# Optimization experiments

Measured on AMD Instinct MI355X. Metric: run time of the kernel, lower is better.

## Reference

```python
import jax, jax.numpy as jnp
import numpy as np

B, D, T, K = 32, 64, 4096, 512
COMMITMENT_COST = 0.25


def setup_inputs() -> dict:
    key = jax.random.key(0)
    k1, k2 = jax.random.split(key)
    z = jax.random.normal(k1, (B, D, T), dtype=jnp.float32)
    # nn.Embedding init: uniform(-1/K, 1/K)
    codebook = jax.random.uniform(k2, (K, D), dtype=jnp.float32,
                                  minval=-1.0 / K, maxval=1.0 / K)
    return {"z": z, "codebook": codebook}


def reference(z, codebook):
    sg = jax.lax.stop_gradient
    zt = jnp.transpose(z, (0, 2, 1))            # [B, T, D]
    zf = zt.reshape(-1, D)                      # [N, D], N = B*T
    # squared L2 distances: ||z||^2 + ||e||^2 - 2 z.e  -> [N, K]
    dists = (jnp.sum(zf * zf, axis=1, keepdims=True)
             + jnp.sum(codebook * codebook, axis=1)
             - 2.0 * jnp.matmul(zf, codebook.T))
    idx = jnp.argmin(dists, axis=1)             # [N]
    # gather codebook rows (same math as one-hot @ codebook)
    quantized = codebook[idx].reshape(zt.shape)  # [B, T, D]
    codebook_loss = jnp.mean((sg(quantized) - zt) ** 2)
    commitment_loss = jnp.mean((quantized - sg(zt)) ** 2)
    vq_loss = codebook_loss + COMMITMENT_COST * commitment_loss
    # straight-through estimator
    quantized_st = zt + sg(quantized - zt)
    quantized_out = jnp.transpose(quantized_st, (0, 2, 1))  # [B, D, T]
    indices = idx.reshape(B, T)
    return vq_loss, quantized_out, indices
```

## Files before the change

### kernel.cpp

```cpp
#include <hip/hip_runtime.h>

#define NB 32
#define ND 64
#define NT 4096
#define NK 512

#define STR 68
#define SM_ZL   0
#define SM_EL   34816
#define SM_ZNL  69632
#define SM_ENL  70144
#define SM_SFIN 70656
#define SM_SRED 71168
#define SM_SIZE 71200

__global__ __launch_bounds__(256) void vq_main(const float* __restrict__ z,
                                               const float* __restrict__ cb,
                                               float* __restrict__ qout,
                                               float* __restrict__ idxout,
                                               double* __restrict__ partials) {
    __shared__ __align__(16) char smem[SM_SIZE];
    float*  zl   = (float*)(smem + SM_ZL);
    float*  el   = (float*)(smem + SM_EL);
    float*  znl  = (float*)(smem + SM_ZNL);
    float*  enl  = (float*)(smem + SM_ENL);
    int*    sfin = (int*)(smem + SM_SFIN);
    double* sred = (double*)(smem + SM_SRED);

    const int bi    = blockIdx.x;
    const int b     = bi >> 5;
    const int tbase = (bi & 31) * 128;
    const int tid   = threadIdx.x;
    const int rg    = tid >> 4;
    const int cg    = tid & 15;

    const size_t zoff = (size_t)b * (ND * NT) + tbase;

#pragma unroll
    for (int j = 0; j < 8; ++j) {
        const int q  = j * 256 + tid;
        const int i4 = q & 31, d = q >> 5;
        const float4 v = *(const float4*)(z + zoff + (size_t)d * NT + i4 * 4);
        const float vv[4] = {v.x, v.y, v.z, v.w};
#pragma unroll
        for (int c = 0; c < 4; ++c) {
            const int r = i4 * 4 + c;
            zl[((r & 7) * 16 + (r >> 3)) * STR + d] = vv[c];
        }
    }
    __syncthreads();

    if (tid < 128) {
        const int r = tid;
        const float4* zr4 = (const float4*)&zl[((r & 7) * 16 + (r >> 3)) * STR];
        float x[64];
#pragma unroll
        for (int w = 0; w < 16; ++w) {
            const float4 t4 = zr4[w];
            x[4*w] = t4.x; x[4*w+1] = t4.y; x[4*w+2] = t4.z; x[4*w+3] = t4.w;
        }
        float r8[8];
#pragma unroll
        for (int jj = 0; jj < 8; ++jj) {
            float s = __fmul_rn(x[jj], x[jj]);
#pragma unroll
            for (int ii = 1; ii < 8; ++ii)
                s = __fadd_rn(s, __fmul_rn(x[8*ii+jj], x[8*ii+jj]));
            r8[jj] = s;
        }
        znl[r] = __fadd_rn(__fadd_rn(__fadd_rn(r8[0],r8[1]), __fadd_rn(r8[2],r8[3])),
                           __fadd_rn(__fadd_rn(r8[4],r8[5]), __fadd_rn(r8[6],r8[7])));
    }
    __syncthreads();

    float znr[8];
#pragma unroll
    for (int i = 0; i < 8; ++i) znr[i] = znl[rg * 8 + i];

    float bst[8]; int bix[8];
#pragma unroll
    for (int i = 0; i < 8; ++i) { bst[i] = __builtin_inff(); bix[i] = 0; }

    for (int cc = 0; cc < 4; ++cc) {
        __syncthreads();
#pragma unroll
        for (int j = 0; j < 8; ++j) {
            const int q  = j * 256 + tid;
            const int kl = q >> 4, d4 = q & 15;
            const float4 v = *(const float4*)(cb + (size_t)(cc * 128 + kl) * ND + d4 * 4);
            *(float4*)&el[((kl & 7) * 16 + (kl >> 3)) * STR + d4 * 4] = v;
        }
        __syncthreads();
        if (tid < 128) {
            const int kl = tid;
            const float* ep = &el[((kl & 7) * 16 + (kl >> 3)) * STR];
            float r8[8];
#pragma unroll
            for (int jj = 0; jj < 8; ++jj) {
                float s = __fmul_rn(ep[jj], ep[jj]);
#pragma unroll
                for (int ii = 1; ii < 8; ++ii)
                    s = __fadd_rn(s, __fmul_rn(ep[8*ii+jj], ep[8*ii+jj]));
                r8[jj] = s;
            }
            enl[kl] = __fadd_rn(__fadd_rn(__fadd_rn(r8[0],r8[1]), __fadd_rn(r8[2],r8[3])),
                                __fadd_rn(__fadd_rn(r8[4],r8[5]), __fadd_rn(r8[6],r8[7])));
        }
        __syncthreads();

        float enr[8];
#pragma unroll
        for (int jj = 0; jj < 8; ++jj) enr[jj] = enl[cg * 8 + jj];

        float acc[8][8];
#pragma unroll
        for (int i = 0; i < 8; ++i)
#pragma unroll
            for (int jj = 0; jj < 8; ++jj) acc[i][jj] = 0.0f;

        const float* zb = zl + rg * STR;
        const float* eb = el + cg * STR;
#pragma unroll 2
        for (int dd = 0; dd < 64; dd += 4) {
            float4 zr[8], er[8];
#pragma unroll
            for (int i = 0; i < 8; ++i)  zr[i]  = *(const float4*)(zb + i  * (16*STR) + dd);
#pragma unroll
            for (int jj = 0; jj < 8; ++jj) er[jj] = *(const float4*)(eb + jj * (16*STR) + dd);
#pragma unroll
            for (int i = 0; i < 8; ++i) {
#pragma unroll
                for (int jj = 0; jj < 8; ++jj) {
                    float a = acc[i][jj];
                    a = __builtin_fmaf(zr[i].x, er[jj].x, a);
                    a = __builtin_fmaf(zr[i].y, er[jj].y, a);
                    a = __builtin_fmaf(zr[i].z, er[jj].z, a);
                    a = __builtin_fmaf(zr[i].w, er[jj].w, a);
                    acc[i][jj] = a;
                }
            }
        }
#pragma unroll
        for (int i = 0; i < 8; ++i) {
#pragma unroll
            for (int jj = 0; jj < 8; ++jj) {
                const float Dv = __fsub_rn(__fadd_rn(znr[i], enr[jj]),
                                           __fmul_rn(2.0f, acc[i][jj]));
                if (Dv < bst[i]) { bst[i] = Dv; bix[i] = cc * 128 + cg * 8 + jj; }
            }
        }
    }

    __syncthreads();
    float* fb = el;
    int*   fi = (int*)(el + 2080);
#pragma unroll
    for (int i = 0; i < 8; ++i) {
        const int r = rg * 8 + i;
        fb[cg * 130 + r] = bst[i];
        fi[cg * 130 + r] = bix[i];
    }
    __syncthreads();
    if (tid < 128) {
        const int r = tid;
        float bb = fb[r]; int bx = fi[r];
#pragma unroll
        for (int c = 1; c < 16; ++c) {
            const float o  = fb[c * 130 + r];
            const int   oi = fi[c * 130 + r];
            if (o < bb || (o == bb && oi < bx)) { bb = o; bx = oi; }
        }
        sfin[r] = bx;
        idxout[(size_t)b * NT + tbase + r] = (float)bx;
    }
    __syncthreads();

    double lsum = 0.0;
#pragma unroll 4
    for (int j = 0; j < 32; ++j) {
        const int q  = j * 256 + tid;
        const int ir = q & 127, d = q >> 7;
        const float zv = zl[((ir & 7) * 16 + (ir >> 3)) * STR + d];
        const float ev = cb[(size_t)sfin[ir] * ND + d];
        const float diff = __fsub_rn(ev, zv);
        qout[(size_t)b * (ND * NT) + (size_t)d * NT + tbase + ir] = __fadd_rn(zv, diff);
        lsum += (double)diff * (double)diff;
    }
#pragma unroll
    for (int off = 32; off > 0; off >>= 1) lsum += __shfl_down(lsum, off, 64);
    if ((tid & 63) == 0) sred[tid >> 6] = lsum;
    __syncthreads();
    if (tid == 0) partials[bi] = (sred[0] + sred[1]) + (sred[2] + sred[3]);
}

__global__ void finalize_kernel(const double* __restrict__ partials,
                                float* __restrict__ out0) {
    __shared__ double sred[4];
    const int tid = threadIdx.x;
    double s = partials[tid] + partials[tid + 256] + partials[tid + 512] + partials[tid + 768];
#pragma unroll
    for (int off = 32; off > 0; off >>= 1) s += __shfl_down(s, off, 64);
    if ((tid & 63) == 0) sred[tid >> 6] = s;
    __syncthreads();
    if (tid == 0) {
        const double m = ((sred[0] + sred[1]) + (sred[2] + sred[3]))
                         / (double)((size_t)NB * NT * ND);
        out0[0] = (float)(1.25 * m);
    }
}

extern "C" void kernel_launch(void* const* d_in, const int* in_sizes, int n_in,
                              void* d_out, int out_size, void* d_ws, size_t ws_size,
                              hipStream_t stream) {
    const float* z  = (const float*)d_in[0];
    const float* cb = (const float*)d_in[1];

    float* out      = (float*)d_out;
    float* loss_out = out;
    float* qout     = out + 1;
    float* idxout   = out + 1 + (size_t)NB * ND * NT;

    double* partials = (double*)d_ws;

    vq_main<<<1024, 256, 0, stream>>>(z, cb, qout, idxout, partials);
    finalize_kernel<<<1, 256, 0, stream>>>(partials, loss_out);
}
```

Before: 200.9 us.

## Use split-bf16 MFMA for distance GEMM with exact fp32 candidate rescoring

Replaces the scalar FP32 distance GEMM with MFMA 32x32x16 bf16 instructions, using a hi/lo bf16 split (three products) to approximate FP32 accuracy. Candidates within a small margin of the running best are recorded per row and rescored exactly in FP32 from global codebook rows to keep argmin matching the reference. Codebook fragment packing and codebook norms move into a separate prep kernel, which removes per-block codebook staging and norm computation. This adds a third launch and carries the risk that the margin is too small, or that the 16-entry candidate cap overflows, which would give wrong indices on near ties.

```diff
diff --git a/kernel.cpp b/kernel.cpp
--- a/kernel.cpp
+++ b/kernel.cpp
@@ -5,59 +5,110 @@
 #define NT 4096
 #define NK 512
 
+typedef __attribute__((ext_vector_type(8))) short short8;
+typedef __attribute__((ext_vector_type(16))) float f32x16;
+typedef unsigned int uint32;
+typedef unsigned short ushort16_t;
+
+#define PERM(r) ((((r) & 7) * 16) + ((r) >> 3))
 #define STR 68
-#define SM_ZL   0
-#define SM_EL   34816
-#define SM_ZNL  69632
-#define SM_ENL  70144
-#define SM_SFIN 70656
-#define SM_SRED 71168
-#define SM_SIZE 71200
-
-__global__ __launch_bounds__(256) void vq_main(const float* __restrict__ z,
-                                               const float* __restrict__ cb,
-                                               float* __restrict__ qout,
-                                               float* __restrict__ idxout,
-                                               double* __restrict__ partials) {
-    __shared__ __align__(16) char smem[SM_SIZE];
-    float*  zl   = (float*)(smem + SM_ZL);
-    float*  el   = (float*)(smem + SM_EL);
-    float*  znl  = (float*)(smem + SM_ZNL);
-    float*  enl  = (float*)(smem + SM_ENL);
-    int*    sfin = (int*)(smem + SM_SFIN);
-    double* sred = (double*)(smem + SM_SRED);
+#define MARGIN 4e-4f
+
+__device__ __forceinline__ ushort16_t bf16rne(float f) {
+    uint32 u = __float_as_uint(f);
+    return (ushort16_t)((u + 0x7FFFu + ((u >> 16) & 1u)) >> 16);
+}
+__device__ __forceinline__ float bf16tof(ushort16_t h) {
+    return __uint_as_float(((uint32)h) << 16);
+}
+
+__global__ void prep_kernel(const float* __restrict__ cb,
+                            uint4* __restrict__ cbfrag,
+                            float* __restrict__ enorm) {
+    const int bi = blockIdx.x, tid = threadIdx.x;
+    if (bi < 16) {
+        const int t = bi * 256 + tid;
+        const int c = t >> 8, rem = t & 255, s = rem >> 6, L = rem & 63;
+        const int kcode = c * 32 + (L & 31);
+        const int dbase = s * 16 + ((L >> 5) << 3);
+        const float* src = cb + (size_t)kcode * 64 + dbase;
+        const float4 pa = *(const float4*)src;
+        const float4 pb = *(const float4*)(src + 4);
+        const float f[8] = {pa.x, pa.y, pa.z, pa.w, pb.x, pb.y, pb.z, pb.w};
+        uint32 hw[4], lw[4];
+#pragma unroll
+        for (int i = 0; i < 4; ++i) {
+            const ushort16_t h0 = bf16rne(f[2*i]);
+            const ushort16_t h1 = bf16rne(f[2*i+1]);
+            const ushort16_t l0 = bf16rne(f[2*i]   - bf16tof(h0));
+            const ushort16_t l1 = bf16rne(f[2*i+1] - bf16tof(h1));
+            hw[i] = (uint32)h0 | ((uint32)h1 << 16);
+            lw[i] = (uint32)l0 | ((uint32)l1 << 16);
+        }
+        cbfrag[(size_t)((c*4+s)*2 + 0)*64 + L] = make_uint4(hw[0],hw[1],hw[2],hw[3]);
+        cbfrag[(size_t)((c*4+s)*2 + 1)*64 + L] = make_uint4(lw[0],lw[1],lw[2],lw[3]);
+    } else {
+        for (int k = tid; k < NK; k += 256) {
+            const float* e = cb + (size_t)k * ND;
+            float r[8];
+#pragma unroll
+            for (int j = 0; j < 8; ++j) {
+                float s = __fmul_rn(e[j], e[j]);
+#pragma unroll
+                for (int i = 1; i < 8; ++i)
+                    s = __fadd_rn(s, __fmul_rn(e[8*i+j], e[8*i+j]));
+                r[j] = s;
+            }
+            enorm[k] = __fadd_rn(__fadd_rn(__fadd_rn(r[0],r[1]), __fadd_rn(r[2],r[3])),
+                                 __fadd_rn(__fadd_rn(r[4],r[5]), __fadd_rn(r[6],r[7])));
+        }
+    }
+}
+
+__global__ __launch_bounds__(256, 3) void vq_main(const float* __restrict__ z,
+                                                  const float* __restrict__ cb,
+                                                  const uint4* __restrict__ cbfrag,
+                                                  const float* __restrict__ enorm,
+                                                  float* __restrict__ qout,
+                                                  float* __restrict__ idxout,
+                                                  double* __restrict__ partials) {
+    __shared__ __align__(16) char smem[46112];
+    float*      zl   = (float*)smem;
+    float*      enl  = (float*)(smem + 34816);
+    float*      znl  = (float*)(smem + 36864);
+    ushort16_t* cand = (ushort16_t*)(smem + 37376);
+    int*        sfin = (int*)(smem + 45568);
+    double*     sred = (double*)(smem + 46080);
 
     const int bi    = blockIdx.x;
     const int b     = bi >> 5;
     const int tbase = (bi & 31) * 128;
     const int tid   = threadIdx.x;
-    const int rg    = tid >> 4;
-    const int cg    = tid & 15;
-
     const size_t zoff = (size_t)b * (ND * NT) + tbase;
 
 #pragma unroll
     for (int j = 0; j < 8; ++j) {
-        const int q  = j * 256 + tid;
-        const int i4 = q & 31, d = q >> 5;
+        const int qq = j * 256 + tid;
+        const int i4 = qq & 31, d = qq >> 5;
         const float4 v = *(const float4*)(z + zoff + (size_t)d * NT + i4 * 4);
         const float vv[4] = {v.x, v.y, v.z, v.w};
 #pragma unroll
         for (int c = 0; c < 4; ++c) {
             const int r = i4 * 4 + c;
-            zl[((r & 7) * 16 + (r >> 3)) * STR + d] = vv[c];
-        }
-    }
+            zl[PERM(r) * STR + d] = vv[c];
+        }
+    }
+    for (int k = tid; k < NK; k += 256) enl[k] = enorm[k];
     __syncthreads();
 
     if (tid < 128) {
         const int r = tid;
-        const float4* zr4 = (const float4*)&zl[((r & 7) * 16 + (r >> 3)) * STR];
+        const float4* zr4 = (const float4*)&zl[PERM(r) * STR];
         float x[64];
 #pragma unroll
-        for (int w = 0; w < 16; ++w) {
-            const float4 t4 = zr4[w];
-            x[4*w] = t4.x; x[4*w+1] = t4.y; x[4*w+2] = t4.z; x[4*w+3] = t4.w;
+        for (int wq = 0; wq < 16; ++wq) {
+            const float4 t4 = zr4[wq];
+            x[4*wq] = t4.x; x[4*wq+1] = t4.y; x[4*wq+2] = t4.z; x[4*wq+3] = t4.w;
         }
         float r8[8];
 #pragma unroll
@@ -71,119 +122,116 @@
         znl[r] = __fadd_rn(__fadd_rn(__fadd_rn(r8[0],r8[1]), __fadd_rn(r8[2],r8[3])),
                            __fadd_rn(__fadd_rn(r8[4],r8[5]), __fadd_rn(r8[6],r8[7])));
     }
-    __syncthreads();
-
-    float znr[8];
-#pragma unroll
-    for (int i = 0; i < 8; ++i) znr[i] = znl[rg * 8 + i];
-
-    float bst[8]; int bix[8];
-#pragma unroll
-    for (int i = 0; i < 8; ++i) { bst[i] = __builtin_inff(); bix[i] = 0; }
-
-    for (int cc = 0; cc < 4; ++cc) {
-        __syncthreads();
-#pragma unroll
-        for (int j = 0; j < 8; ++j) {
-            const int q  = j * 256 + tid;
-            const int kl = q >> 4, d4 = q & 15;
-            const float4 v = *(const float4*)(cb + (size_t)(cc * 128 + kl) * ND + d4 * 4);
-            *(float4*)&el[((kl & 7) * 16 + (kl >> 3)) * STR + d4 * 4] = v;
-        }
-        __syncthreads();
-        if (tid < 128) {
-            const int kl = tid;
-            const float* ep = &el[((kl & 7) * 16 + (kl >> 3)) * STR];
-            float r8[8];
-#pragma unroll
-            for (int jj = 0; jj < 8; ++jj) {
-                float s = __fmul_rn(ep[jj], ep[jj]);
-#pragma unroll
-                for (int ii = 1; ii < 8; ++ii)
-                    s = __fadd_rn(s, __fmul_rn(ep[8*ii+jj], ep[8*ii+jj]));
-                r8[jj] = s;
+
+    const int L    = tid & 63;
+    const int w    = tid >> 6;
+    const int h    = L >> 5;
+    const int rowl = w * 32 + (L & 31);
+    short8 bhf[4], blf[4];
+    {
+        const float* zrow = &zl[PERM(rowl) * STR];
+#pragma unroll
+        for (int s = 0; s < 4; ++s) {
+            const int d0 = s * 16 + h * 8;
+            const float4 pa = *(const float4*)(zrow + d0);
+            const float4 pb = *(const float4*)(zrow + d0 + 4);
+            const float f[8] = {pa.x, pa.y, pa.z, pa.w, pb.x, pb.y, pb.z, pb.w};
+            uint32 hw[4], lw[4];
+#pragma unroll
+            for (int i = 0; i < 4; ++i) {
+                const ushort16_t h0 = bf16rne(f[2*i]);
+                const ushort16_t h1 = bf16rne(f[2*i+1]);
+                const ushort16_t l0 = bf16rne(f[2*i]   - bf16tof(h0));
+                const ushort16_t l1 = bf16rne(f[2*i+1] - bf16tof(h1));
+                hw[i] = (uint32)h0 | ((uint32)h1 << 16);
+                lw[i] = (uint32)l0 | ((uint32)l1 << 16);
             }
-            enl[kl] = __fadd_rn(__fadd_rn(__fadd_rn(r8[0],r8[1]), __fadd_rn(r8[2],r8[3])),
-                                __fadd_rn(__fadd_rn(r8[4],r8[5]), __fadd_rn(r8[6],r8[7])));
-        }
-        __syncthreads();
-
-        float enr[8];
-#pragma unroll
-        for (int jj = 0; jj < 8; ++jj) enr[jj] = enl[cg * 8 + jj];
-
-        float acc[8][8];
-#pragma unroll
-        for (int i = 0; i < 8; ++i)
-#pragma unroll
-            for (int jj = 0; jj < 8; ++jj) acc[i][jj] = 0.0f;
-
-        const float* zb = zl + rg * STR;
-        const float* eb = el + cg * STR;
-#pragma unroll 2
-        for (int dd = 0; dd < 64; dd += 4) {
-            float4 zr[8], er[8];
-#pragma unroll
-            for (int i = 0; i < 8; ++i)  zr[i]  = *(const float4*)(zb + i  * (16*STR) + dd);
-#pragma unroll
-            for (int jj = 0; jj < 8; ++jj) er[jj] = *(const float4*)(eb + jj * (16*STR) + dd);
-#pragma unroll
-            for (int i = 0; i < 8; ++i) {
-#pragma unroll
-                for (int jj = 0; jj < 8; ++jj) {
-                    float a = acc[i][jj];
-                    a = __builtin_fmaf(zr[i].x, er[jj].x, a);
-                    a = __builtin_fmaf(zr[i].y, er[jj].y, a);
-                    a = __builtin_fmaf(zr[i].z, er[jj].z, a);
-                    a = __builtin_fmaf(zr[i].w, er[jj].w, a);
-                    acc[i][jj] = a;
-                }
-            }
-        }
-#pragma unroll
-        for (int i = 0; i < 8; ++i) {
-#pragma unroll
-            for (int jj = 0; jj < 8; ++jj) {
-                const float Dv = __fsub_rn(__fadd_rn(znr[i], enr[jj]),
-                                           __fmul_rn(2.0f, acc[i][jj]));
-                if (Dv < bst[i]) { bst[i] = Dv; bix[i] = cc * 128 + cg * 8 + jj; }
-            }
-        }
-    }
-
-    __syncthreads();
-    float* fb = el;
-    int*   fi = (int*)(el + 2080);
-#pragma unroll
-    for (int i = 0; i < 8; ++i) {
-        const int r = rg * 8 + i;
-        fb[cg * 130 + r] = bst[i];
-        fi[cg * 130 + r] = bix[i];
-    }
-    __syncthreads();
-    if (tid < 128) {
-        const int r = tid;
-        float bb = fb[r]; int bx = fi[r];
-#pragma unroll
-        for (int c = 1; c < 16; ++c) {
-            const float o  = fb[c * 130 + r];
-            const int   oi = fi[c * 130 + r];
-            if (o < bb || (o == bb && oi < bx)) { bb = o; bx = oi; }
-        }
-        sfin[r] = bx;
-        idxout[(size_t)b * NT + tbase + r] = (float)bx;
+            union { uint4 u; short8 s8; } uh, ul;
+            uh.u = make_uint4(hw[0],hw[1],hw[2],hw[3]);
+            ul.u = make_uint4(lw[0],lw[1],lw[2],lw[3]);
+            bhf[s] = uh.s8; blf[s] = ul.s8;
+        }
+    }
+    __syncthreads();
+
+    float best  = __builtin_inff();
+    int   bestk = 0;
+    int   cnt   = 0;
+    ushort16_t* mylist = cand + (rowl * 2 + h) * 16;
+
+    for (int c = 0; c < 16; ++c) {
+        union { uint4 u; short8 s8; } ah[4], al[4];
+#pragma unroll
+        for (int s = 0; s < 4; ++s) {
+            ah[s].u = cbfrag[(size_t)((c*4+s)*2 + 0)*64 + L];
+            al[s].u = cbfrag[(size_t)((c*4+s)*2 + 1)*64 + L];
+        }
+        f32x16 acc;
+#pragma unroll
+        for (int r = 0; r < 16; ++r) acc[r] = 0.0f;
+#pragma unroll
+        for (int s = 0; s < 4; ++s) {
+            acc = __builtin_amdgcn_mfma_f32_32x32x16_bf16(ah[s].s8, bhf[s], acc, 0, 0, 0);
+            acc = __builtin_amdgcn_mfma_f32_32x32x16_bf16(al[s].s8, bhf[s], acc, 0, 0, 0);
+            acc = __builtin_amdgcn_mfma_f32_32x32x16_bf16(ah[s].s8, blf[s], acc, 0, 0, 0);
+        }
+#pragma unroll
+        for (int r = 0; r < 16; ++r) {
+            const int kc = c * 32 + ((r & 3) + 8 * (r >> 2) + 4 * h);
+            const float en = enl[kc];
+            const float sv = __builtin_fmaf(-2.0f, acc[r], en);
+            if (sv < best) { best = sv; bestk = kc; }
+            if (sv <= best + MARGIN && cnt < 16) { mylist[cnt] = (ushort16_t)kc; ++cnt; }
+        }
+    }
+
+    float x[64];
+    {
+        const float4* zr4 = (const float4*)&zl[PERM(rowl) * STR];
+#pragma unroll
+        for (int i = 0; i < 16; ++i) {
+            const float4 t4 = zr4[i];
+            x[4*i] = t4.x; x[4*i+1] = t4.y; x[4*i+2] = t4.z; x[4*i+3] = t4.w;
+        }
+    }
+    const float zn = znl[rowl];
+    float bd; int bk = bestk;
+    {
+        const float* e = cb + (size_t)bestk * ND;
+        float a = 0.0f;
+#pragma unroll
+        for (int d = 0; d < 64; ++d) a = __builtin_fmaf(x[d], e[d], a);
+        bd = __fsub_rn(__fadd_rn(zn, enl[bestk]), __fmul_rn(2.0f, a));
+    }
+    for (int i = 0; i < cnt; ++i) {
+        const int k2 = mylist[i];
+        const float* e = cb + (size_t)k2 * ND;
+        float a = 0.0f;
+#pragma unroll
+        for (int d = 0; d < 64; ++d) a = __builtin_fmaf(x[d], e[d], a);
+        const float dv = __fsub_rn(__fadd_rn(zn, enl[k2]), __fmul_rn(2.0f, a));
+        if (dv < bd || (dv == bd && k2 < bk)) { bd = dv; bk = k2; }
+    }
+    {
+        const float obd = __shfl_xor(bd, 32);
+        const int   obk = __shfl_xor(bk, 32);
+        if (obd < bd || (obd == bd && obk < bk)) { bd = obd; bk = obk; }
+    }
+    if (h == 0) {
+        sfin[rowl] = bk;
+        idxout[(size_t)b * NT + tbase + rowl] = (float)bk;
     }
     __syncthreads();
 
     double lsum = 0.0;
 #pragma unroll 4
     for (int j = 0; j < 32; ++j) {
-        const int q  = j * 256 + tid;
-        const int ir = q & 127, d = q >> 7;
-        const float zv = zl[((ir & 7) * 16 + (ir >> 3)) * STR + d];
+        const int qq = j * 256 + tid;
+        const int ir = qq & 127, d = qq >> 7;
+        const float zv = zl[PERM(ir) * STR + d];
         const float ev = cb[(size_t)sfin[ir] * ND + d];
         const float diff = __fsub_rn(ev, zv);
-        qout[(size_t)b * (ND * NT) + (size_t)d * NT + tbase + ir] = __fadd_rn(zv, diff);
+        qout[(size_t)b * (ND*NT) + (size_t)d * NT + tbase + ir] = __fadd_rn(zv, diff);
         lsum += (double)diff * (double)diff;
     }
 #pragma unroll
@@ -220,8 +268,11 @@
     float* qout     = out + 1;
     float* idxout   = out + 1 + (size_t)NB * ND * NT;
 
-    double* partials = (double*)d_ws;
-
-    vq_main<<<1024, 256, 0, stream>>>(z, cb, qout, idxout, partials);
+    uint4*  cbfrag   = (uint4*)d_ws;
+    float*  enorm    = (float*)((char*)d_ws + 131072);
+    double* partials = (double*)((char*)d_ws + 133120);
+
+    prep_kernel<<<17, 256, 0, stream>>>(cb, cbfrag, enorm);
+    vq_main<<<1024, 256, 0, stream>>>(z, cb, cbfrag, enorm, qout, idxout, partials);
     finalize_kernel<<<1, 256, 0, stream>>>(partials, loss_out);
 }
```

Measured after the change: 218.1 us. 8.5% more time.
